# Performance work log

Measured on AMD Instinct MI355X. Metric: run time of the kernel, lower is better.

## Reference

```python
import jax, jax.numpy as jnp
import numpy as np


def setup_inputs() -> dict:
    key = jax.random.key(0)
    ks = jax.random.split(key, 4)
    B, Tq, Tv = 8, 1024, 1024
    Dq, Dv, Do = 1024, 1024, 1024
    scale_q = 1.0 / np.sqrt(Dq)
    scale_2 = 1.0 / np.sqrt(Dq + Dv)
    return {
        "query": jax.random.normal(ks[0], (B, Tq, Dq), jnp.float32),
        "values": jax.random.normal(ks[1], (B, Tv, Dv), jnp.float32),
        "W1": jax.random.normal(ks[2], (Dv, Dq), jnp.float32) * scale_q,
        "b1": jnp.zeros((Dv,), jnp.float32),
        "W2": jax.random.normal(ks[3], (Do, Dq + Dv), jnp.float32) * scale_2,
        "b2": jnp.zeros((Do,), jnp.float32),
    }


def reference(query, values, W1, b1, W2, b2):
    # linear1: project query into values space  [B, Tq, Dv]
    q_resize = jnp.einsum("btd,vd->btv", query, W1) + b1
    # attention scores [B, Tq, Tv] and softmax over keys
    scores = jnp.einsum("bqd,bkd->bqk", q_resize, values)
    attn = jax.nn.softmax(scores, axis=-1)
    # attended values [B, Tq, Dv]
    attended = jnp.einsum("bqk,bkd->bqd", attn, values)
    # concat + linear2 + tanh
    feed = jnp.concatenate([attended, query], axis=-1)
    out = jnp.tanh(jnp.einsum("btf,of->bto", feed, W2) + b2)
    return out
```

## Files before the change

kernel.cpp:

```cpp
#include <hip/hip_runtime.h>
#include <hip/hip_bf16.h>

typedef __bf16 bf16x8 __attribute__((ext_vector_type(8)));
typedef float f32x4 __attribute__((ext_vector_type(4)));
typedef unsigned short u16;
typedef unsigned short us4 __attribute__((ext_vector_type(4)));
typedef unsigned int u32;

__device__ __forceinline__ u16 f2bf(float x) {
  union { float f; u32 u; } v; v.f = x;
  u32 r = v.u + 0x7FFFu + ((v.u >> 16) & 1u);
  return (u16)(r >> 16);
}
__device__ __forceinline__ float bf2f(u16 h) {
  union { u32 u; float f; } v; v.u = ((u32)h) << 16;
  return v.f;
}

__device__ __forceinline__ void glds16(const void* g, void* l) {
  __builtin_amdgcn_global_load_lds(
      (const __attribute__((address_space(1))) void*)g,
      (__attribute__((address_space(3))) void*)l, 16, 0, 0);
}

template<int NSEG, int EPI>
__global__ __launch_bounds__(256)
void gemm_bt(const u16* __restrict__ A, const u16* __restrict__ B,
             void* __restrict__ Cout, const float* __restrict__ bias,
             int K0, int lda, int ldb, int ldc,
             long sA, long sB, long sC)
{
  __shared__ __align__(16) u16 As[128 * 32];
  __shared__ __align__(16) u16 Bs[128 * 32];

  const int bz   = blockIdx.z;
  const int brow = blockIdx.x * 128;
  const int bcol = blockIdx.y * 128;
  const int tid  = threadIdx.x;
  const int wid  = tid >> 6;
  const int lane = tid & 63;
  const int wr   = wid >> 1, wc = wid & 1;

  const u16* Ab = A + (long)bz * sA + (long)brow * lda;
  const u16* Bb = B + (long)bz * sB + (long)bcol * ldb;

  f32x4 acc[4][4];
#pragma unroll
  for (int m = 0; m < 4; ++m)
#pragma unroll
    for (int n = 0; n < 4; ++n) acc[m][n] = (f32x4){0.f, 0.f, 0.f, 0.f};

  const int srow = wid * 32 + (lane >> 2);
  const int scol = (lane & 3) * 8;
  u16* lA0 = As + wid * 32 * 32;
  u16* lA1 = lA0 + 16 * 32;
  u16* lB0 = Bs + wid * 32 * 32;
  u16* lB1 = lB0 + 16 * 32;

  const int lr = lane & 15;
  const int lk = (lane >> 4) * 8;

  for (int seg = 0; seg < NSEG; ++seg) {
    const u16* Aseg = Ab + ((NSEG == 3 && seg == 1) ? K0 : 0);
    const u16* Bseg = Bb + ((NSEG == 3 && seg == 2) ? K0 : 0);
    for (int kt = 0; kt < K0; kt += 32) {
      const u16* ga = Aseg + (long)srow * lda + kt + scol;
      const u16* gb = Bseg + (long)srow * ldb + kt + scol;
      glds16(ga, lA0);
      glds16(ga + (long)16 * lda, lA1);
      glds16(gb, lB0);
      glds16(gb + (long)16 * ldb, lB1);
      __syncthreads();

      bf16x8 af[4], bfr[4];
#pragma unroll
      for (int m = 0; m < 4; ++m)
        af[m] = *(const bf16x8*)(As + (wr * 64 + m * 16 + lr) * 32 + lk);
#pragma unroll
      for (int n = 0; n < 4; ++n)
        bfr[n] = *(const bf16x8*)(Bs + (wc * 64 + n * 16 + lr) * 32 + lk);
#pragma unroll
      for (int m = 0; m < 4; ++m)
#pragma unroll
        for (int n = 0; n < 4; ++n)
          acc[m][n] = __builtin_amdgcn_mfma_f32_16x16x32_bf16(af[m], bfr[n], acc[m][n], 0, 0, 0);
      __syncthreads();
    }
  }

  const int crow0 = brow + wr * 64;
  const int ccol0 = bcol + wc * 64;
  const int orow  = (lane >> 4) * 4;
  const int ocol  = lane & 15;

#pragma unroll
  for (int m = 0; m < 4; ++m) {
#pragma unroll
    for (int n = 0; n < 4; ++n) {
      const int col = ccol0 + n * 16 + ocol;
      float bv = 0.f;
      if (EPI == 1 || EPI == 3) bv = bias[col];
#pragma unroll
      for (int j = 0; j < 4; ++j) {
        const int row = crow0 + m * 16 + orow + j;
        float v = acc[m][n][j] + bv;
        if (EPI == 0) {
          ((float*)Cout)[(long)bz * sC + (long)row * ldc + col] = v;
        } else if (EPI == 1) {
          u16 hi = f2bf(v);
          u16 lo = f2bf(v - bf2f(hi));
          u16* Co = (u16*)Cout + (long)bz * sC + (long)row * ldc;
          Co[col] = hi;
          Co[col + 1024] = lo;
        } else if (EPI == 2) {
          ((u16*)Cout)[(long)bz * sC + (long)row * ldc + col] = f2bf(v);
        } else {
          ((float*)Cout)[(long)bz * sC + (long)row * ldc + col] = tanhf(v);
        }
      }
    }
  }
}

__global__ __launch_bounds__(256)
void split_pack(const float* __restrict__ X, u16* __restrict__ P,
                u16* __restrict__ FQ, long n4)
{
  long i = (long)blockIdx.x * 256 + threadIdx.x;
  const long stride = (long)gridDim.x * 256;
  for (; i < n4; i += stride) {
    float4 x = ((const float4*)X)[i];
    long e = i * 4;
    long row = e >> 10;
    int col = (int)(e & 1023);
    float xs[4] = {x.x, x.y, x.z, x.w};
    u16 h[4], l[4];
#pragma unroll
    for (int j = 0; j < 4; ++j) {
      h[j] = f2bf(xs[j]);
      l[j] = f2bf(xs[j] - bf2f(h[j]));
    }
    us4 hv = {h[0], h[1], h[2], h[3]};
    us4 lv = {l[0], l[1], l[2], l[3]};
    *(us4*)(P + row * 2048 + col) = hv;
    *(us4*)(P + row * 2048 + 1024 + col) = lv;
    if (FQ) *(us4*)(FQ + row * 2048 + 1024 + col) = hv;
  }
}

__global__ __launch_bounds__(256)
void conv_values(const float* __restrict__ V, u16* __restrict__ Vp,
                 u16* __restrict__ VT)
{
  __shared__ u16 tile[64][68];
  const int b  = blockIdx.z;
  const int d0 = blockIdx.x * 64;
  const int k0 = blockIdx.y * 64;
  const int t  = threadIdx.x;
  const int tr = t >> 4;
  const int tc = (t & 15) * 4;
  const float* Vb = V + (long)b * (1024L * 1024);
  u16* Vpb = Vp + (long)b * (1024L * 2048);
  u16* VTb = VT + (long)b * (1024L * 1024);

#pragma unroll
  for (int i = 0; i < 4; ++i) {
    int k = tr + i * 16;
    float4 x = *(const float4*)(Vb + (long)(k0 + k) * 1024 + d0 + tc);
    float xs[4] = {x.x, x.y, x.z, x.w};
    u16 h[4], l[4];
#pragma unroll
    for (int j = 0; j < 4; ++j) {
      h[j] = f2bf(xs[j]);
      l[j] = f2bf(xs[j] - bf2f(h[j]));
      tile[k][tc + j] = h[j];
    }
    us4 hv = {h[0], h[1], h[2], h[3]};
    us4 lv = {l[0], l[1], l[2], l[3]};
    *(us4*)(Vpb + (long)(k0 + k) * 2048 + d0 + tc) = hv;
    *(us4*)(Vpb + (long)(k0 + k) * 2048 + 1024 + d0 + tc) = lv;
  }
  __syncthreads();
#pragma unroll
  for (int i = 0; i < 4; ++i) {
    int d = tr + i * 16;
    int k = tc;
    us4 o = {tile[k][d], tile[k + 1][d], tile[k + 2][d], tile[k + 3][d]};
    *(us4*)(VTb + (long)(d0 + d) * 1024 + k0 + k) = o;
  }
}

__global__ __launch_bounds__(256)
void conv_cast(const float* __restrict__ X, u16* __restrict__ Y, long n4)
{
  long i = (long)blockIdx.x * 256 + threadIdx.x;
  const long stride = (long)gridDim.x * 256;
  for (; i < n4; i += stride) {
    float4 x = ((const float4*)X)[i];
    us4 o = {f2bf(x.x), f2bf(x.y), f2bf(x.z), f2bf(x.w)};
    *(us4*)(Y + i * 4) = o;
  }
}

__global__ __launch_bounds__(256)
void softmax_rows(const float* __restrict__ S, u16* __restrict__ A)
{
  const long row = blockIdx.x;
  const float* src = S + row * 1024;
  const int t = threadIdx.x;
  const int lane = t & 63, wid = t >> 6;
  float4 v = ((const float4*)src)[t];
  float m = fmaxf(fmaxf(v.x, v.y), fmaxf(v.z, v.w));
#pragma unroll
  for (int off = 32; off >= 1; off >>= 1)
    m = fmaxf(m, __shfl_xor(m, off));
  __shared__ float redm[4];
  if (lane == 0) redm[wid] = m;
  __syncthreads();
  m = fmaxf(fmaxf(redm[0], redm[1]), fmaxf(redm[2], redm[3]));
  float e0 = __expf(v.x - m), e1 = __expf(v.y - m);
  float e2 = __expf(v.z - m), e3 = __expf(v.w - m);
  float s = e0 + e1 + e2 + e3;
#pragma unroll
  for (int off = 32; off >= 1; off >>= 1)
    s += __shfl_xor(s, off);
  __shared__ float reds[4];
  if (lane == 0) reds[wid] = s;
  __syncthreads();
  s = reds[0] + reds[1] + reds[2] + reds[3];
  float inv = 1.0f / s;
  us4 o = {f2bf(e0 * inv), f2bf(e1 * inv), f2bf(e2 * inv), f2bf(e3 * inv)};
  ((us4*)(A + row * 1024))[t] = o;
}

extern "C" void kernel_launch(void* const* d_in, const int* in_sizes, int n_in,
                              void* d_out, int out_size, void* d_ws, size_t ws_size,
                              hipStream_t stream)
{
  const float* query  = (const float*)d_in[0];
  const float* values = (const float*)d_in[1];
  const float* W1     = (const float*)d_in[2];
  const float* b1     = (const float*)d_in[3];
  const float* W2     = (const float*)d_in[4];
  const float* b2     = (const float*)d_in[5];
  float* out = (float*)d_out;

  char* ws = (char*)d_ws;
  const long MB = 1024L * 1024;
  u16*   W1p    = (u16*)(ws);
  u16*   W2b    = (u16*)(ws + 4 * MB);
  u16*   Aq     = (u16*)(ws + 8 * MB);
  float* scores = (float*)(ws + 8 * MB);
  u16*   qr     = (u16*)(ws + 40 * MB);
  u16*   attn   = (u16*)(ws + 40 * MB);
  u16*   Vp     = (u16*)(ws + 72 * MB);
  u16*   VT     = (u16*)(ws + 104 * MB);
  u16*   feed   = (u16*)(ws + 120 * MB);

  split_pack<<<dim3(2048), dim3(256), 0, stream>>>(query, Aq, feed, (8192L * 1024) / 4);
  split_pack<<<dim3(1024), dim3(256), 0, stream>>>(W1, W1p, (u16*)nullptr, (1024L * 1024) / 4);
  conv_values<<<dim3(16, 16, 8), dim3(256), 0, stream>>>(values, Vp, VT);
  conv_cast<<<dim3(1024), dim3(256), 0, stream>>>(W2, W2b, (1024L * 2048) / 4);

  gemm_bt<3, 1><<<dim3(64, 8, 1), dim3(256), 0, stream>>>(
      Aq, W1p, qr, b1, 1024, 2048, 2048, 2048, 0L, 0L, 0L);

  gemm_bt<3, 0><<<dim3(8, 8, 8), dim3(256), 0, stream>>>(
      qr, Vp, scores, (const float*)nullptr, 1024, 2048, 2048, 1024,
      1024L * 2048, 1024L * 2048, 1024L * 1024);

  softmax_rows<<<dim3(8192), dim3(256), 0, stream>>>(scores, attn);

  gemm_bt<1, 2><<<dim3(8, 8, 8), dim3(256), 0, stream>>>(
      attn, VT, feed, (const float*)nullptr, 1024, 1024, 1024, 2048,
      1024L * 1024, 1024L * 1024, 1024L * 2048);

  gemm_bt<1, 3><<<dim3(64, 8, 1), dim3(256), 0, stream>>>(
      feed, W2b, out, b2, 2048, 2048, 2048, 1024, 0L, 0L, 0L);
}
```

Before: 391.1 us.

## Double-buffer GEMM LDS tiles with 256x128 blocks, 512 threads and XCD-aware tile swizzle

The GEMM kernel now issues the global-to-LDS loads for the next 64-wide K step while computing the current one, using double-buffered LDS and one barrier per step. Each block covers 256x128 with 8 waves, and the grid is flattened to 256 blocks with a block-index swizzle that groups neighbouring tiles onto the same XCD. The aim is to hide memory latency, halve barrier count, improve L2 reuse and match one block per CU. The cost is more LDS per block (96KB) and lower occupancy. Correctness relies on the in-flight async LDS loads being finished at the single barrier.

```diff
diff --git a/kernel.cpp b/kernel.cpp
--- a/kernel.cpp
+++ b/kernel.cpp
@@ -24,22 +24,30 @@
 }
 
 template<int NSEG, int EPI>
-__global__ __launch_bounds__(256)
+__global__ __launch_bounds__(512)
 void gemm_bt(const u16* __restrict__ A, const u16* __restrict__ B,
              void* __restrict__ Cout, const float* __restrict__ bias,
              int K0, int lda, int ldb, int ldc,
-             long sA, long sB, long sC)
-{
-  __shared__ __align__(16) u16 As[128 * 32];
-  __shared__ __align__(16) u16 Bs[128 * 32];
-
-  const int bz   = blockIdx.z;
-  const int brow = blockIdx.x * 128;
-  const int bcol = blockIdx.y * 128;
+             long sA, long sB, long sC, int nx, int ny)
+{
+  __shared__ __align__(16) u16 As[2][2][256 * 32];
+  __shared__ __align__(16) u16 Bs[2][2][128 * 32];
+
+  const int d = blockIdx.x;
+  const int L = ((d & 7) << 5) | (d >> 3);
+  const int nxy = nx * ny;
+  const int bz = L / nxy;
+  const int rr = L - bz * nxy;
+  const int bx = rr / ny;
+  const int by = rr - bx * ny;
+  const int brow = bx * 256;
+  const int bcol = by * 128;
+
   const int tid  = threadIdx.x;
   const int wid  = tid >> 6;
   const int lane = tid & 63;
-  const int wr   = wid >> 1, wc = wid & 1;
+  const int wr   = wid >> 1;
+  const int wc   = wid & 1;
 
   const u16* Ab = A + (long)bz * sA + (long)brow * lda;
   const u16* Bb = B + (long)bz * sB + (long)bcol * ldb;
@@ -50,42 +58,60 @@
 #pragma unroll
     for (int n = 0; n < 4; ++n) acc[m][n] = (f32x4){0.f, 0.f, 0.f, 0.f};
 
-  const int srow = wid * 32 + (lane >> 2);
-  const int scol = (lane & 3) * 8;
-  u16* lA0 = As + wid * 32 * 32;
-  u16* lA1 = lA0 + 16 * 32;
-  u16* lB0 = Bs + wid * 32 * 32;
-  u16* lB1 = lB0 + 16 * 32;
+  const int sr = lane >> 2;
+  const int sc = (lane & 3) * 8;
+
+  const int ksteps = (NSEG == 3) ? 16 : (K0 >> 6);
+  const int NT = NSEG * ksteps;
+
+  auto stage = [&](int buf, int t) {
+    int seg, kt;
+    if (NSEG == 3) { seg = t >> 4; kt = (t & 15) << 6; }
+    else           { seg = 0;      kt = t << 6; }
+    const u16* Aseg = Ab + ((NSEG == 3 && seg == 1) ? K0 : 0) + kt;
+    const u16* Bseg = Bb + ((NSEG == 3 && seg == 2) ? K0 : 0) + kt;
+#pragma unroll
+    for (int h = 0; h < 2; ++h) {
+#pragma unroll
+      for (int i = 0; i < 2; ++i) {
+        const int row = wid * 32 + i * 16;
+        glds16(Aseg + (long)(row + sr) * lda + h * 32 + sc,
+               As[buf][h] + row * 32);
+      }
+      {
+        const int row = wid * 16;
+        glds16(Bseg + (long)(row + sr) * ldb + h * 32 + sc,
+               Bs[buf][h] + row * 32);
+      }
+    }
+  };
 
   const int lr = lane & 15;
   const int lk = (lane >> 4) * 8;
 
-  for (int seg = 0; seg < NSEG; ++seg) {
-    const u16* Aseg = Ab + ((NSEG == 3 && seg == 1) ? K0 : 0);
-    const u16* Bseg = Bb + ((NSEG == 3 && seg == 2) ? K0 : 0);
-    for (int kt = 0; kt < K0; kt += 32) {
-      const u16* ga = Aseg + (long)srow * lda + kt + scol;
-      const u16* gb = Bseg + (long)srow * ldb + kt + scol;
-      glds16(ga, lA0);
-      glds16(ga + (long)16 * lda, lA1);
-      glds16(gb, lB0);
-      glds16(gb + (long)16 * ldb, lB1);
-      __syncthreads();
-
+  stage(0, 0);
+  __syncthreads();
+
+  int buf = 0;
+  for (int t = 0; t < NT; ++t) {
+    if (t + 1 < NT) stage(buf ^ 1, t + 1);
+#pragma unroll
+    for (int h = 0; h < 2; ++h) {
       bf16x8 af[4], bfr[4];
 #pragma unroll
       for (int m = 0; m < 4; ++m)
-        af[m] = *(const bf16x8*)(As + (wr * 64 + m * 16 + lr) * 32 + lk);
+        af[m] = *(const bf16x8*)(As[buf][h] + (wr * 64 + m * 16 + lr) * 32 + lk);
 #pragma unroll
       for (int n = 0; n < 4; ++n)
-        bfr[n] = *(const bf16x8*)(Bs + (wc * 64 + n * 16 + lr) * 32 + lk);
+        bfr[n] = *(const bf16x8*)(Bs[buf][h] + (wc * 64 + n * 16 + lr) * 32 + lk);
 #pragma unroll
       for (int m = 0; m < 4; ++m)
 #pragma unroll
         for (int n = 0; n < 4; ++n)
           acc[m][n] = __builtin_amdgcn_mfma_f32_16x16x32_bf16(af[m], bfr[n], acc[m][n], 0, 0, 0);
-      __syncthreads();
-    }
+    }
+    __syncthreads();
+    buf ^= 1;
   }
 
   const int crow0 = brow + wr * 64;
@@ -262,19 +288,19 @@
   conv_values<<<dim3(16, 16, 8), dim3(256), 0, stream>>>(values, Vp, VT);
   conv_cast<<<dim3(1024), dim3(256), 0, stream>>>(W2, W2b, (1024L * 2048) / 4);
 
-  gemm_bt<3, 1><<<dim3(64, 8, 1), dim3(256), 0, stream>>>(
-      Aq, W1p, qr, b1, 1024, 2048, 2048, 2048, 0L, 0L, 0L);
-
-  gemm_bt<3, 0><<<dim3(8, 8, 8), dim3(256), 0, stream>>>(
+  gemm_bt<3, 1><<<dim3(256), dim3(512), 0, stream>>>(
+      Aq, W1p, qr, b1, 1024, 2048, 2048, 2048, 0L, 0L, 0L, 32, 8);
+
+  gemm_bt<3, 0><<<dim3(256), dim3(512), 0, stream>>>(
       qr, Vp, scores, (const float*)nullptr, 1024, 2048, 2048, 1024,
-      1024L * 2048, 1024L * 2048, 1024L * 1024);
+      1024L * 2048, 1024L * 2048, 1024L * 1024, 4, 8);
 
   softmax_rows<<<dim3(8192), dim3(256), 0, stream>>>(scores, attn);
 
-  gemm_bt<1, 2><<<dim3(8, 8, 8), dim3(256), 0, stream>>>(
+  gemm_bt<1, 2><<<dim3(256), dim3(512), 0, stream>>>(
       attn, VT, feed, (const float*)nullptr, 1024, 1024, 1024, 2048,
-      1024L * 1024, 1024L * 1024, 1024L * 2048);
-
-  gemm_bt<1, 3><<<dim3(64, 8, 1), dim3(256), 0, stream>>>(
-      feed, W2b, out, b2, 2048, 2048, 2048, 1024, 0L, 0L, 0L);
-}
+      1024L * 1024, 1024L * 1024, 1024L * 2048, 4, 8);
+
+  gemm_bt<1, 3><<<dim3(256), dim3(512), 0, stream>>>(
+      feed, W2b, out, b2, 2048, 2048, 2048, 1024, 0L, 0L, 0L, 32, 8);
+}
```

Measured after the change: 390.6 us. About the same (-0.1%).

## Replace GEMMs with 256x256 pipelined split-K kernel using atomic accumulation

Applied to the files above, without the earlier changes.

Replaces the 128x128 single-buffered GEMM with a 512-thread 256x256 tile kernel. It uses a 4-slot LDS ring filled by global_load_lds with two tiles prefetched ahead, XCD-aware block remapping, and split-K across blocks with atomic float adds into zeroed buffers. Bias, hi/lo split and tanh move into separate elementwise passes (repack_qr, final_tanh). This aims for more data reuse per tile, overlap of loads with MFMA, and full occupancy of the CUs at low block counts. The cost is extra memsets, atomics and elementwise passes over 32MB buffers.

```diff
diff --git a/kernel.cpp b/kernel.cpp
--- a/kernel.cpp
+++ b/kernel.cpp
@@ -24,98 +24,140 @@
 }
 
 template<int NSEG, int EPI>
-__global__ __launch_bounds__(256)
-void gemm_bt(const u16* __restrict__ A, const u16* __restrict__ B,
-             void* __restrict__ Cout, const float* __restrict__ bias,
-             int K0, int lda, int ldb, int ldc,
-             long sA, long sB, long sC)
-{
-  __shared__ __align__(16) u16 As[128 * 32];
-  __shared__ __align__(16) u16 Bs[128 * 32];
-
-  const int bz   = blockIdx.z;
-  const int brow = blockIdx.x * 128;
-  const int bcol = blockIdx.y * 128;
+__global__ __launch_bounds__(512, 1)
+void gemm256(const u16* __restrict__ A, const u16* __restrict__ B,
+             void* __restrict__ Cout, int K0, int lda, int ldb, int ldc,
+             long sA, long sB, long sC,
+             int nb, int nx, int ny, int tpz)
+{
+  __shared__ __align__(1024) u16 lds[4][2][8192];
+
+  const int d = blockIdx.x;
+  const int Lx = (d & 7) * ((int)gridDim.x >> 3) + (d >> 3);
+  int tmp = Lx;
+  const int by = tmp % ny; tmp /= ny;
+  const int bx = tmp % nx; tmp /= nx;
+  const int bz = tmp % nb; tmp /= nb;
+  const int kz = tmp;
+
+  const int brow = bx * 256;
+  const int bcol = by * 256;
+
   const int tid  = threadIdx.x;
   const int wid  = tid >> 6;
   const int lane = tid & 63;
-  const int wr   = wid >> 1, wc = wid & 1;
+  const int wrm  = wid >> 2;
+  const int wcn  = wid & 3;
 
   const u16* Ab = A + (long)bz * sA + (long)brow * lda;
   const u16* Bb = B + (long)bz * sB + (long)bcol * ldb;
 
-  f32x4 acc[4][4];
-#pragma unroll
-  for (int m = 0; m < 4; ++m)
+  f32x4 acc[8][4];
+#pragma unroll
+  for (int m = 0; m < 8; ++m)
 #pragma unroll
     for (int n = 0; n < 4; ++n) acc[m][n] = (f32x4){0.f, 0.f, 0.f, 0.f};
 
-  const int srow = wid * 32 + (lane >> 2);
+  const int r15 = lane & 15;
+  const int laneRd = ((r15 >> 1) * 64) + ((r15 & 1) * 32) + ((lane >> 4) * 8);
+
+  const int srow = ((lane >> 3) * 2) + ((lane & 7) >> 2);
   const int scol = (lane & 3) * 8;
-  u16* lA0 = As + wid * 32 * 32;
-  u16* lA1 = lA0 + 16 * 32;
-  u16* lB0 = Bs + wid * 32 * 32;
-  u16* lB1 = lB0 + 16 * 32;
-
-  const int lr = lane & 15;
-  const int lk = (lane >> 4) * 8;
-
-  for (int seg = 0; seg < NSEG; ++seg) {
-    const u16* Aseg = Ab + ((NSEG == 3 && seg == 1) ? K0 : 0);
-    const u16* Bseg = Bb + ((NSEG == 3 && seg == 2) ? K0 : 0);
-    for (int kt = 0; kt < K0; kt += 32) {
-      const u16* ga = Aseg + (long)srow * lda + kt + scol;
-      const u16* gb = Bseg + (long)srow * ldb + kt + scol;
-      glds16(ga, lA0);
-      glds16(ga + (long)16 * lda, lA1);
-      glds16(gb, lB0);
-      glds16(gb + (long)16 * ldb, lB1);
-      __syncthreads();
-
-      bf16x8 af[4], bfr[4];
-#pragma unroll
-      for (int m = 0; m < 4; ++m)
-        af[m] = *(const bf16x8*)(As + (wr * 64 + m * 16 + lr) * 32 + lk);
-#pragma unroll
-      for (int n = 0; n < 4; ++n)
-        bfr[n] = *(const bf16x8*)(Bs + (wc * 64 + n * 16 + lr) * 32 + lk);
-#pragma unroll
-      for (int m = 0; m < 4; ++m)
+
+  auto srcAB = [&](int t, const u16*& Aseg, const u16*& Bseg) {
+    int seg, kte;
+    if (NSEG == 3) { seg = t >> 5; kte = (t & 31) << 5; }
+    else           { seg = 0;      kte = t << 5; }
+    Aseg = Ab + ((NSEG == 3 && seg == 1) ? K0 : 0) + kte;
+    Bseg = Bb + ((NSEG == 3 && seg == 2) ? K0 : 0) + kte;
+  };
+  auto stage2 = [&](const u16* base, int ld, u16* dstOp) {
+#pragma unroll
+    for (int q = 0; q < 2; ++q) {
+      const int rowbase = wid * 32 + q * 16;
+      glds16(base + (long)(rowbase + srow) * ld + scol,
+             dstOp + (rowbase >> 1) * 64);
+    }
+  };
+
+  const int t0 = kz * tpz;
+
+  {
+    const u16 *As, *Bs;
+    srcAB(t0, As, Bs);
+    stage2(As, lda, lds[0][0]);
+    stage2(Bs, ldb, lds[0][1]);
+    srcAB(t0 + 1, As, Bs);
+    stage2(As, lda, lds[1][0]);
+    stage2(Bs, ldb, lds[1][1]);
+  }
+  asm volatile("s_waitcnt vmcnt(4)" ::: "memory");
+  __builtin_amdgcn_s_barrier();
+
+  for (int tau = 0; tau < tpz; ++tau) {
+    const u16* LA = lds[tau & 3][0];
+    const u16* LB = lds[tau & 3][1];
+    const bool pre = (tau + 2 < tpz);
+    const u16 *Asg = nullptr, *Bsg = nullptr;
+    u16 *LAs = nullptr, *LBs = nullptr;
+    if (pre) {
+      srcAB(t0 + tau + 2, Asg, Bsg);
+      LAs = lds[(tau + 2) & 3][0];
+      LBs = lds[(tau + 2) & 3][1];
+    }
+
+    bf16x8 bv[4];
+#pragma unroll
+    for (int p = 0; p < 2; ++p) {
+      bf16x8 av[4];
+#pragma unroll
+      for (int j = 0; j < 4; ++j)
+        av[j] = *(const bf16x8*)(LA + (wrm * 128 + (p * 4 + j) * 16) * 32 + laneRd);
+      if (p == 0) {
 #pragma unroll
         for (int n = 0; n < 4; ++n)
-          acc[m][n] = __builtin_amdgcn_mfma_f32_16x16x32_bf16(af[m], bfr[n], acc[m][n], 0, 0, 0);
-      __syncthreads();
-    }
-  }
-
-  const int crow0 = brow + wr * 64;
-  const int ccol0 = bcol + wc * 64;
+          bv[n] = *(const bf16x8*)(LB + (wcn * 64 + n * 16) * 32 + laneRd);
+        if (pre) stage2(Asg, lda, LAs);
+      } else {
+        if (pre) stage2(Bsg, ldb, LBs);
+      }
+      __builtin_amdgcn_s_barrier();
+      asm volatile("s_waitcnt lgkmcnt(0)" ::: "memory");
+      __builtin_amdgcn_sched_barrier(0);
+      __builtin_amdgcn_s_setprio(1);
+#pragma unroll
+      for (int j = 0; j < 4; ++j)
+#pragma unroll
+        for (int n = 0; n < 4; ++n)
+          acc[p * 4 + j][n] = __builtin_amdgcn_mfma_f32_16x16x32_bf16(
+              av[j], bv[n], acc[p * 4 + j][n], 0, 0, 0);
+      __builtin_amdgcn_s_setprio(0);
+      if (p == 1) {
+        if (pre) { asm volatile("s_waitcnt vmcnt(4)" ::: "memory"); }
+        else     { asm volatile("s_waitcnt vmcnt(0)" ::: "memory"); }
+      }
+      __builtin_amdgcn_sched_barrier(0);
+      __builtin_amdgcn_s_barrier();
+    }
+  }
+
+  const int crow0 = brow + wrm * 128;
+  const int ccol0 = bcol + wcn * 64;
   const int orow  = (lane >> 4) * 4;
   const int ocol  = lane & 15;
-
-#pragma unroll
-  for (int m = 0; m < 4; ++m) {
+#pragma unroll
+  for (int m = 0; m < 8; ++m) {
 #pragma unroll
     for (int n = 0; n < 4; ++n) {
       const int col = ccol0 + n * 16 + ocol;
-      float bv = 0.f;
-      if (EPI == 1 || EPI == 3) bv = bias[col];
 #pragma unroll
       for (int j = 0; j < 4; ++j) {
         const int row = crow0 + m * 16 + orow + j;
-        float v = acc[m][n][j] + bv;
+        const float v = acc[m][n][j];
         if (EPI == 0) {
-          ((float*)Cout)[(long)bz * sC + (long)row * ldc + col] = v;
-        } else if (EPI == 1) {
-          u16 hi = f2bf(v);
-          u16 lo = f2bf(v - bf2f(hi));
-          u16* Co = (u16*)Cout + (long)bz * sC + (long)row * ldc;
-          Co[col] = hi;
-          Co[col + 1024] = lo;
-        } else if (EPI == 2) {
+          unsafeAtomicAdd(&((float*)Cout)[(long)bz * sC + (long)row * ldc + col], v);
+        } else {
           ((u16*)Cout)[(long)bz * sC + (long)row * ldc + col] = f2bf(v);
-        } else {
-          ((float*)Cout)[(long)bz * sC + (long)row * ldc + col] = tanhf(v);
         }
       }
     }
@@ -145,6 +187,54 @@
     *(us4*)(P + row * 2048 + col) = hv;
     *(us4*)(P + row * 2048 + 1024 + col) = lv;
     if (FQ) *(us4*)(FQ + row * 2048 + 1024 + col) = hv;
+  }
+}
+
+__global__ __launch_bounds__(256)
+void repack_qr(const float* __restrict__ P, const float* __restrict__ b1,
+               u16* __restrict__ qr, long n4)
+{
+  long i = (long)blockIdx.x * 256 + threadIdx.x;
+  const long stride = (long)gridDim.x * 256;
+  for (; i < n4; i += stride) {
+    float4 a = ((const float4*)P)[i];
+    long e = i * 4;
+    long row = e >> 10;
+    int col = (int)(e & 1023);
+    float xs[4];
+    xs[0] = a.x + b1[col];
+    xs[1] = a.y + b1[col + 1];
+    xs[2] = a.z + b1[col + 2];
+    xs[3] = a.w + b1[col + 3];
+    u16 h[4], l[4];
+#pragma unroll
+    for (int j = 0; j < 4; ++j) {
+      h[j] = f2bf(xs[j]);
+      l[j] = f2bf(xs[j] - bf2f(h[j]));
+    }
+    us4 hv = {h[0], h[1], h[2], h[3]};
+    us4 lv = {l[0], l[1], l[2], l[3]};
+    *(us4*)(qr + row * 2048 + col) = hv;
+    *(us4*)(qr + row * 2048 + 1024 + col) = lv;
+  }
+}
+
+__global__ __launch_bounds__(256)
+void final_tanh(const float* __restrict__ P, const float* __restrict__ b2,
+                float* __restrict__ out, long n4)
+{
+  long i = (long)blockIdx.x * 256 + threadIdx.x;
+  const long stride = (long)gridDim.x * 256;
+  for (; i < n4; i += stride) {
+    float4 a = ((const float4*)P)[i];
+    long e = i * 4;
+    int col = (int)(e & 1023);
+    float4 o;
+    o.x = tanhf(a.x + b2[col]);
+    o.y = tanhf(a.y + b2[col + 1]);
+    o.z = tanhf(a.z + b2[col + 2]);
+    o.w = tanhf(a.w + b2[col + 3]);
+    ((float4*)out)[i] = o;
   }
 }
 
@@ -183,10 +273,10 @@
   __syncthreads();
 #pragma unroll
   for (int i = 0; i < 4; ++i) {
-    int d = tr + i * 16;
+    int dd = tr + i * 16;
     int k = tc;
-    us4 o = {tile[k][d], tile[k + 1][d], tile[k + 2][d], tile[k + 3][d]};
-    *(us4*)(VTb + (long)(d0 + d) * 1024 + k0 + k) = o;
+    us4 o = {tile[k][dd], tile[k + 1][dd], tile[k + 2][dd], tile[k + 3][dd]};
+    *(us4*)(VTb + (long)(d0 + dd) * 1024 + k0 + k) = o;
   }
 }
 
@@ -250,31 +340,38 @@
   u16*   W1p    = (u16*)(ws);
   u16*   W2b    = (u16*)(ws + 4 * MB);
   u16*   Aq     = (u16*)(ws + 8 * MB);
-  float* scores = (float*)(ws + 8 * MB);
+  float* Psc    = (float*)(ws + 8 * MB);
   u16*   qr     = (u16*)(ws + 40 * MB);
   u16*   attn   = (u16*)(ws + 40 * MB);
   u16*   Vp     = (u16*)(ws + 72 * MB);
   u16*   VT     = (u16*)(ws + 104 * MB);
   u16*   feed   = (u16*)(ws + 120 * MB);
-
-  split_pack<<<dim3(2048), dim3(256), 0, stream>>>(query, Aq, feed, (8192L * 1024) / 4);
+  float* Pout   = out;
+
+  const long N8M = 8388608;
+
+  split_pack<<<dim3(2048), dim3(256), 0, stream>>>(query, Aq, feed, N8M / 4);
   split_pack<<<dim3(1024), dim3(256), 0, stream>>>(W1, W1p, (u16*)nullptr, (1024L * 1024) / 4);
   conv_values<<<dim3(16, 16, 8), dim3(256), 0, stream>>>(values, Vp, VT);
   conv_cast<<<dim3(1024), dim3(256), 0, stream>>>(W2, W2b, (1024L * 2048) / 4);
 
-  gemm_bt<3, 1><<<dim3(64, 8, 1), dim3(256), 0, stream>>>(
-      Aq, W1p, qr, b1, 1024, 2048, 2048, 2048, 0L, 0L, 0L);
-
-  gemm_bt<3, 0><<<dim3(8, 8, 8), dim3(256), 0, stream>>>(
-      qr, Vp, scores, (const float*)nullptr, 1024, 2048, 2048, 1024,
-      1024L * 2048, 1024L * 2048, 1024L * 1024);
-
-  softmax_rows<<<dim3(8192), dim3(256), 0, stream>>>(scores, attn);
-
-  gemm_bt<1, 2><<<dim3(8, 8, 8), dim3(256), 0, stream>>>(
-      attn, VT, feed, (const float*)nullptr, 1024, 1024, 1024, 2048,
-      1024L * 1024, 1024L * 1024, 1024L * 2048);
-
-  gemm_bt<1, 3><<<dim3(64, 8, 1), dim3(256), 0, stream>>>(
-      feed, W2b, out, b2, 2048, 2048, 2048, 1024, 0L, 0L, 0L);
-}
+  hipMemsetAsync(Pout, 0, N8M * 4, stream);
+  gemm256<3, 0><<<dim3(256), dim3(512), 0, stream>>>(
+      Aq, W1p, Pout, 1024, 2048, 2048, 1024, 0L, 0L, 0L, 1, 32, 4, 48);
+  repack_qr<<<dim3(2048), dim3(256), 0, stream>>>(Pout, b1, qr, N8M / 4);
+
+  hipMemsetAsync(Psc, 0, N8M * 4, stream);
+  gemm256<3, 0><<<dim3(256), dim3(512), 0, stream>>>(
+      qr, Vp, Psc, 1024, 2048, 2048, 1024, 1024L * 2048, 1024L * 2048,
+      1024L * 1024, 8, 4, 4, 48);
+  softmax_rows<<<dim3(8192), dim3(256), 0, stream>>>(Psc, attn);
+
+  gemm256<1, 2><<<dim3(128), dim3(512), 0, stream>>>(
+      attn, VT, feed, 1024, 1024, 1024, 2048, 1024L * 1024, 1024L * 1024,
+      1024L * 2048, 8, 4, 4, 32);
+
+  hipMemsetAsync(Pout, 0, N8M * 4, stream);
+  gemm256<1, 0><<<dim3(256), dim3(512), 0, stream>>>(
+      feed, W2b, Pout, 2048, 2048, 2048, 1024, 0L, 0L, 0L, 1, 32, 4, 32);
+  final_tanh<<<dim3(2048), dim3(256), 0, stream>>>(Pout, b2, out, N8M / 4);
+}
```

Result: slower. 505.2 us (+29.2%).
